# Kernel tuning notes

Measured on AMD Instinct MI355X. Metric: run time of the kernel, lower is better.

The kernel has to match this reference:

```python
import jax, jax.numpy as jnp
import numpy as np

EPS = 1e-5
NUM_HEADS = 4
HEAD_DIM = 64
NUM_STEPS = 3


def layernorm(x, g, b):
    mu = jnp.mean(x, axis=-1, keepdims=True)
    var = jnp.mean((x - mu) ** 2, axis=-1, keepdims=True)
    return (x - mu) / jnp.sqrt(var + EPS) * g + b


def entmax15(x):
    # exact alpha=1.5 entmax along last axis (Peters et al. 2019)
    n = x.shape[-1]
    x = x - jnp.max(x, axis=-1, keepdims=True)
    x = x / 2.0
    srt = -jnp.sort(-x, axis=-1)                      # descending
    rho = jnp.arange(1, n + 1, dtype=x.dtype)
    cs = jnp.cumsum(srt, axis=-1)
    cs2 = jnp.cumsum(srt * srt, axis=-1)
    mean = cs / rho
    ss = cs2 - mean * cs                              # k * (mean_sq - mean^2)
    delta = (1.0 - ss) / rho
    d = jnp.clip(delta, 0.0)
    safe = jnp.where(d > 0, d, 1.0)
    tau = mean - jnp.where(d > 0, jnp.sqrt(safe), 0.0)
    support = (tau <= srt).astype(jnp.int32)
    k_star = jnp.sum(support, axis=-1, keepdims=True) - 1
    tau_star = jnp.take_along_axis(tau, k_star, axis=-1)
    p = jnp.clip(x - tau_star, 0.0)
    return p * p


def setup_inputs() -> dict:
    key = jax.random.key(0)
    ks = jax.random.split(key, 8)
    B, S, Dh = 2, 512, 2048
    N, Dm = 8192, 1024
    T = NUM_HEADS * HEAD_DIM  # 256
    hidden = jax.random.normal(ks[0], (B, S, Dh), dtype=jnp.float32)
    memory = jax.random.normal(ks[1], (N, Dm), dtype=jnp.float32)
    Wq = jax.random.normal(ks[2], (Dh, T), dtype=jnp.float32) * 0.02
    Wk = jax.random.normal(ks[3], (Dm, T), dtype=jnp.float32) * 0.02
    Wv = jax.random.normal(ks[4], (Dm, T), dtype=jnp.float32) * 0.02
    Wo = jax.random.normal(ks[5], (T, Dh), dtype=jnp.float32) * 0.02
    log_beta = jnp.full((NUM_HEADS,), float(np.log(1.0 / np.sqrt(HEAD_DIM))), dtype=jnp.float32)
    g_s = jnp.ones((Dh,), jnp.float32)
    b_s = jnp.zeros((Dh,), jnp.float32)
    g_m = jnp.ones((Dm,), jnp.float32)
    b_m = jnp.zeros((Dm,), jnp.float32)
    return {"hidden": hidden, "memory": memory, "Wq": Wq, "Wk": Wk, "Wv": Wv,
            "Wo": Wo, "log_beta": log_beta, "g_s": g_s, "b_s": b_s,
            "g_m": g_m, "b_m": b_m}


def reference(hidden, memory, Wq, Wk, Wv, Wo, log_beta, g_s, b_s, g_m, b_m):
    B, S, _ = hidden.shape
    N = memory.shape[0]
    H, D = NUM_HEADS, HEAD_DIM
    Q = layernorm(hidden, g_s, b_s) @ Wq                         # [B,S,H*D]
    mem_n = layernorm(memory, g_m, b_m)
    K = (mem_n @ Wk).reshape(N, H, D).transpose(1, 0, 2)         # [H,N,D]
    V = (mem_n @ Wv).reshape(N, H, D).transpose(1, 0, 2)         # [H,N,D]
    xi = Q.reshape(B, S, H, D).transpose(0, 2, 1, 3)             # [B,H,S,D]
    beta = jnp.exp(log_beta)[None, :, None, None]                # [1,H,1,1]
    for _ in range(NUM_STEPS):
        scores = jnp.einsum('bhsd,hnd->bhsn', xi, K) * beta      # [B,H,S,N]
        w = entmax15(scores)
        xi = jnp.einsum('bhsn,hnd->bhsd', w, V)
    converged = xi.transpose(0, 2, 1, 3).reshape(B, S, H * D)
    output = converged @ Wo                                      # [B,S,hidden_dim]
    return output, converged
```

## Files before the change

kernel.cpp:

```cpp
#include <hip/hip_runtime.h>
#include <math.h>

typedef _Float16 f16;
typedef f16 f16x8 __attribute__((ext_vector_type(8)));
typedef float f32x4 __attribute__((ext_vector_type(4)));

#define QSCALE 16384.0f
#define QINV 6.103515625e-5f
#define QOFF 2.5f

__device__ __forceinline__ float wred_add(float v) {
#pragma unroll
  for (int off = 32; off >= 1; off >>= 1) v += __shfl_xor(v, off, 64);
  return v;
}
__device__ __forceinline__ float wred_max(float v) {
#pragma unroll
  for (int off = 32; off >= 1; off >>= 1) v = fmaxf(v, __shfl_xor(v, off, 64));
  return v;
}

__global__ __launch_bounds__(256) void ln_stats_all_kernel(
    const float* __restrict__ hidden, const float* __restrict__ memory,
    float* __restrict__ mu_h, float* __restrict__ rs_h,
    float* __restrict__ mu_m, float* __restrict__ rs_m) {
  int b = blockIdx.x, tid = threadIdx.x;
  const float* X;
  float* mu;
  float* rs;
  int cols, row;
  if (b < 1024) { X = hidden; cols = 2048; mu = mu_h; rs = rs_h; row = b; }
  else { X = memory; cols = 1024; mu = mu_m; rs = rs_m; row = b - 1024; }
  const float4* xr = (const float4*)(X + (size_t)row * cols);
  int nv = cols >> 10;
  float s = 0.f, s2 = 0.f;
  for (int v = 0; v < nv; ++v) {
    float4 x4 = xr[tid + (v << 8)];
    s += x4.x + x4.y + x4.z + x4.w;
    s2 += x4.x * x4.x + x4.y * x4.y + x4.z * x4.z + x4.w * x4.w;
  }
  s = wred_add(s);
  s2 = wred_add(s2);
  __shared__ float rb[8];
  int wid = tid >> 6, lane = tid & 63;
  if (lane == 0) { rb[wid] = s; rb[4 + wid] = s2; }
  __syncthreads();
  if (tid == 0) {
    float S = rb[0] + rb[1] + rb[2] + rb[3];
    float S2 = rb[4] + rb[5] + rb[6] + rb[7];
    float m = S / (float)cols;
    float var = S2 / (float)cols - m * m;
    mu[row] = m;
    rs[row] = 1.f / sqrtf(var + 1e-5f);
  }
}

__global__ __launch_bounds__(256) void split_a_kernel(
    const float* __restrict__ X, const float* __restrict__ mu,
    const float* __restrict__ rs, f16x8* __restrict__ Ah,
    f16x8* __restrict__ Al, int M, int Kd, int lay) {
  int blk = blockIdx.x * 4 + (threadIdx.x >> 6);
  int l = threadIdx.x & 63;
  int nmt = M >> 4;
  int kc = blk / nmt, mt = blk - kc * nmt;
  int m = mt * 16 + (l & 15);
  int k = kc * 32 + ((l >> 4) << 3);
  const float* src;
  if (lay == 0) {
    src = X + (size_t)m * Kd + k;
  } else {
    int b = m >> 9, s = m & 511, hh = k >> 6, d = k & 63;
    src = X + ((((size_t)b * 4 + hh) * 512 + s) << 6) + d;
  }
  float mm = mu ? mu[m] : 0.f;
  float rr = rs ? rs[m] : 1.f;
  f16x8 hi, lo;
#pragma unroll
  for (int j = 0; j < 8; ++j) {
    float v = (src[j] - mm) * rr;
    f16 hv = (f16)v;
    hi[j] = hv;
    lo[j] = (f16)((v - (float)hv) * 512.f);
  }
  size_t o = ((size_t)blk << 6) + l;
  Ah[o] = hi;
  Al[o] = lo;
}

__global__ __launch_bounds__(256) void split_w_all_kernel(
    const float* __restrict__ Wq, const float* __restrict__ Wk,
    const float* __restrict__ Wv, const float* __restrict__ Wo,
    const float* __restrict__ g_s, const float* __restrict__ g_m,
    f16x8* __restrict__ Bqh, f16x8* __restrict__ Bql,
    f16x8* __restrict__ Bkh, f16x8* __restrict__ Bkl,
    f16x8* __restrict__ Bvh, f16x8* __restrict__ Bvl,
    f16x8* __restrict__ Boh, f16x8* __restrict__ Bol) {
  int b = blockIdx.x;
  const float* W;
  const float* g;
  f16x8 *Bh, *Bl;
  int N, base;
  if (b < 256) { W = Wq; g = g_s; Bh = Bqh; Bl = Bql; N = 256; base = 0; }
  else if (b < 384) { W = Wk; g = g_m; Bh = Bkh; Bl = Bkl; N = 256; base = 256; }
  else if (b < 512) { W = Wv; g = g_m; Bh = Bvh; Bl = Bvl; N = 256; base = 384; }
  else { W = Wo; g = nullptr; Bh = Boh; Bl = Bol; N = 2048; base = 512; }
  int blk = (b - base) * 4 + (threadIdx.x >> 6);
  int l = threadIdx.x & 63;
  int nnt = N >> 4;
  int kc = blk / nnt, nt = blk - kc * nnt;
  int n = nt * 16 + (l & 15);
  int k0 = kc * 32 + ((l >> 4) << 3);
  f16x8 hi, lo;
#pragma unroll
  for (int j = 0; j < 8; ++j) {
    float v = W[(size_t)(k0 + j) * N + n];
    if (g) v *= g[k0 + j];
    f16 hv = (f16)v;
    hi[j] = hv;
    lo[j] = (f16)((v - (float)hv) * 512.f);
  }
  size_t o = ((size_t)blk << 6) + l;
  Bh[o] = hi;
  Bl[o] = lo;
}

__global__ __launch_bounds__(256) void wcol3_kernel(
    const float* __restrict__ Wq, const float* __restrict__ bq,
    const float* __restrict__ Wk, const float* __restrict__ bk,
    const float* __restrict__ Wv, const float* __restrict__ bv,
    float* __restrict__ vbq, float* __restrict__ vbk,
    float* __restrict__ vbv) {
  int which = blockIdx.z;
  const float* W = which == 0 ? Wq : (which == 1 ? Wk : Wv);
  const float* b = which == 0 ? bq : (which == 1 ? bk : bv);
  float* vb = which == 0 ? vbq : (which == 1 ? vbk : vbv);
  int Kd = which == 0 ? 2048 : 1024;
  int t = threadIdx.x;
  int kpb = Kd >> 4;
  int k0 = blockIdx.y * kpb;
  float s = 0.f;
  for (int k = k0; k < k0 + kpb; ++k) s = fmaf(b[k], W[(size_t)k * 256 + t], s);
  atomicAdd(&vb[t], s);
}

__global__ __launch_bounds__(256) void gemm_mfma_kernel(
    const f16x8* __restrict__ Ah, const f16x8* __restrict__ Al,
    const f16x8* __restrict__ Bh, const f16x8* __restrict__ Bl,
    const float* __restrict__ vb, float* __restrict__ outf,
    f16x8* __restrict__ o16a, f16x8* __restrict__ o16b, int M, int N, int nk,
    int out_mode) {
  __shared__ __align__(16) float Ts[64][68];
  const int tid = threadIdx.x;
  const int w = tid >> 6, l = tid & 63;
  const int ql = l & 15, g = l >> 4;
  const int bn = blockIdx.x, bm = blockIdx.y;
  const size_t astr = ((size_t)(M >> 4)) << 6;
  const size_t bstr = ((size_t)(N >> 4)) << 6;
  const f16x8* aph = Ah + (((size_t)(bm * 4 + w)) << 6) + l;
  const f16x8* apl = Al + (((size_t)(bm * 4 + w)) << 6) + l;
  const f16x8* bph = Bh + (((size_t)(bn * 4)) << 6) + l;
  const f16x8* bpl = Bl + (((size_t)(bn * 4)) << 6) + l;

  f32x4 cm[4], cx[4];
#pragma unroll
  for (int nf = 0; nf < 4; ++nf) {
    cm[nf] = (f32x4){0.f, 0.f, 0.f, 0.f};
    cx[nf] = (f32x4){0.f, 0.f, 0.f, 0.f};
  }

  f16x8 a0h = aph[0], a0l = apl[0];
  f16x8 b0h[4], b0l[4];
#pragma unroll
  for (int nf = 0; nf < 4; ++nf) {
    b0h[nf] = bph[nf << 6];
    b0l[nf] = bpl[nf << 6];
  }

  for (int kc = 0; kc < nk - 1; ++kc) {
    const size_t ao = (size_t)(kc + 1) * astr;
    const size_t bo = (size_t)(kc + 1) * bstr;
    f16x8 a1h = aph[ao], a1l = apl[ao];
    f16x8 b1h[4], b1l[4];
#pragma unroll
    for (int nf = 0; nf < 4; ++nf) {
      b1h[nf] = bph[bo + (nf << 6)];
      b1l[nf] = bpl[bo + (nf << 6)];
    }
#pragma unroll
    for (int nf = 0; nf < 4; ++nf) {
      cm[nf] = __builtin_amdgcn_mfma_f32_16x16x32_f16(a0h, b0h[nf], cm[nf], 0, 0, 0);
      cx[nf] = __builtin_amdgcn_mfma_f32_16x16x32_f16(a0h, b0l[nf], cx[nf], 0, 0, 0);
      cx[nf] = __builtin_amdgcn_mfma_f32_16x16x32_f16(a0l, b0h[nf], cx[nf], 0, 0, 0);
    }
    a0h = a1h;
    a0l = a1l;
#pragma unroll
    for (int nf = 0; nf < 4; ++nf) {
      b0h[nf] = b1h[nf];
      b0l[nf] = b1l[nf];
    }
  }
#pragma unroll
  for (int nf = 0; nf < 4; ++nf) {
    cm[nf] = __builtin_amdgcn_mfma_f32_16x16x32_f16(a0h, b0h[nf], cm[nf], 0, 0, 0);
    cx[nf] = __builtin_amdgcn_mfma_f32_16x16x32_f16(a0h, b0l[nf], cx[nf], 0, 0, 0);
    cx[nf] = __builtin_amdgcn_mfma_f32_16x16x32_f16(a0l, b0h[nf], cx[nf], 0, 0, 0);
  }

  float vbc[4] = {0.f, 0.f, 0.f, 0.f};
  if (vb) {
#pragma unroll
    for (int nf = 0; nf < 4; ++nf) vbc[nf] = vb[bn * 64 + nf * 16 + ql];
  }

  if (out_mode == 0) {
#pragma unroll
    for (int nf = 0; nf < 4; ++nf)
#pragma unroll
      for (int r = 0; r < 4; ++r) {
        float val = fmaf(cx[nf][r], 0.001953125f, cm[nf][r]) + vbc[nf];
        int m = bm * 64 + w * 16 + (g << 2) + r;
        int n = bn * 64 + nf * 16 + ql;
        int b = m >> 9, s = m & 511, hh = n >> 6, d = n & 63;
        outf[((((size_t)b * 4 + hh) * 512 + s) << 6) + d] = val;
      }
  } else if (out_mode == 3) {
#pragma unroll
    for (int nf = 0; nf < 4; ++nf)
#pragma unroll
      for (int r = 0; r < 4; ++r) {
        float val = fmaf(cx[nf][r], 0.001953125f, cm[nf][r]) + vbc[nf];
        int m = bm * 64 + w * 16 + (g << 2) + r;
        int n = bn * 64 + nf * 16 + ql;
        outf[(size_t)m * N + n] = val;
      }
  } else {
#pragma unroll
    for (int nf = 0; nf < 4; ++nf)
#pragma unroll
      for (int r = 0; r < 4; ++r)
        Ts[w * 16 + (g << 2) + r][nf * 16 + ql] =
            fmaf(cx[nf][r], 0.001953125f, cm[nf][r]) + vbc[nf];
    __syncthreads();
    if (out_mode == 4) {
#pragma unroll
      for (int i = 0; i < 2; ++i) {
        int slot = tid + (i << 8);
        int blk = slot >> 6, l2 = slot & 63;
        int ktl = blk >> 1, dc = blk & 1;
        int key = (ktl << 4) + (l2 & 15);
        int db = (dc << 5) + ((l2 >> 4) << 3);
        f16x8 hi, lo;
#pragma unroll
        for (int j = 0; j < 8; ++j) {
          float v = Ts[key][db + j];
          f16 hv = (f16)v;
          hi[j] = hv;
          lo[j] = (f16)((v - (float)hv) * 512.f);
        }
        size_t o = (((size_t)(bn * 512 + bm * 4 + ktl) * 2 + dc) << 6) + l2;
        o16a[o] = hi;
        o16b[o] = lo;
      }
    } else {
#pragma unroll
      for (int i = 0; i < 2; ++i) {
        int slot = tid + (i << 8);
        int blk = slot >> 6, l2 = slot & 63;
        int dt = blk >> 1, kcl = blk & 1;
        int keyb = (kcl << 5) + ((l2 >> 4) << 3);
        int d = (dt << 4) + (l2 & 15);
        f16x8 v8;
#pragma unroll
        for (int j = 0; j < 8; ++j) v8[j] = (f16)Ts[keyb + j][d];
        size_t o = (((size_t)(bn * 4 + dt) * 256 + bm * 2 + kcl) << 6) + l2;
        o16a[o] = v8;
      }
    }
  }
}

__global__ __launch_bounds__(512) void hop_score_kernel(
    const float* __restrict__ xi_in, const f16x8* __restrict__ Khi,
    const f16x8* __restrict__ Klo, const float* __restrict__ log_beta,
    unsigned short* __restrict__ Y) {
  __shared__ float xiq[16][64];
  __shared__ float mxb[8][16];
  __shared__ float mxs[16];
  const int tid = threadIdx.x;
  const int w = tid >> 6, l = tid & 63;
  const int ql = l & 15, g = l >> 4;
  const int bh = blockIdx.x & 7, qtile = blockIdx.x >> 3;
  const int h = bh & 3;
  const size_t base_io = ((size_t)bh * 512 + qtile * 16) * 64;

  float beta = expf(log_beta[h]);
  for (int i = tid; i < 1024; i += 512)
    xiq[i >> 6][i & 63] = xi_in[base_io + i] * beta;
  __syncthreads();

  f16x8 xh0, xh1, xl0, xl1;
#pragma unroll
  for (int j = 0; j < 8; ++j) {
    float x0 = xiq[ql][(g << 3) + j];
    float x1 = xiq[ql][32 + (g << 3) + j];
    f16 h0 = (f16)x0, h1 = (f16)x1;
    xh0[j] = h0; xl0[j] = (f16)((x0 - (float)h0) * 512.f);
    xh1[j] = h1; xl1[j] = (f16)((x1 - (float)h1) * 512.f);
  }

  const f16x8* kb = Khi + (size_t)h * 65536 + l;
  const f16x8* kl = Klo + (size_t)h * 65536 + l;
  const int kt0 = w * 64;

  float mymax = -3.4e38f;
  for (int kt = kt0; kt < kt0 + 2; ++kt) {
    f32x4 c = {0.f, 0.f, 0.f, 0.f};
    c = __builtin_amdgcn_mfma_f32_16x16x32_f16(kb[(size_t)kt * 128], xh0, c, 0, 0, 0);
    c = __builtin_amdgcn_mfma_f32_16x16x32_f16(kb[(size_t)kt * 128 + 64], xh1, c, 0, 0, 0);
    mymax = fmaxf(fmaxf(fmaxf(c[0], c[1]), fmaxf(c[2], c[3])), mymax);
  }
  mymax = fmaxf(mymax, __shfl_xor(mymax, 16, 64));
  mymax = fmaxf(mymax, __shfl_xor(mymax, 32, 64));
  if (l < 16) mxb[w][ql] = mymax;
  __syncthreads();
  if (tid < 16) {
    float m = mxb[0][tid];
#pragma unroll
    for (int ww = 1; ww < 8; ++ww) m = fmaxf(m, mxb[ww][tid]);
    mxs[tid] = m;
  }
  __syncthreads();
  const float mh = mxs[ql] * 0.5f;
  const float qc = QOFF * QSCALE + 0.5f - mh * QSCALE;

  const size_t Ybase = (size_t)(bh * 32 + qtile) * 131072;
  for (int kt = kt0; kt < kt0 + 64; ++kt) {
    f16x8 a0 = kb[(size_t)kt * 128], a1 = kb[(size_t)kt * 128 + 64];
    f16x8 b0 = kl[(size_t)kt * 128], b1 = kl[(size_t)kt * 128 + 64];
    f32x4 cm = {0.f, 0.f, 0.f, 0.f}, cx = {0.f, 0.f, 0.f, 0.f};
    cm = __builtin_amdgcn_mfma_f32_16x16x32_f16(a0, xh0, cm, 0, 0, 0);
    cm = __builtin_amdgcn_mfma_f32_16x16x32_f16(a1, xh1, cm, 0, 0, 0);
    cx = __builtin_amdgcn_mfma_f32_16x16x32_f16(b0, xh0, cx, 0, 0, 0);
    cx = __builtin_amdgcn_mfma_f32_16x16x32_f16(a0, xl0, cx, 0, 0, 0);
    cx = __builtin_amdgcn_mfma_f32_16x16x32_f16(b1, xh1, cx, 0, 0, 0);
    cx = __builtin_amdgcn_mfma_f32_16x16x32_f16(a1, xl1, cx, 0, 0, 0);
    ushort4 uv;
    unsigned short* up = (unsigned short*)&uv;
#pragma unroll
    for (int r = 0; r < 4; ++r) {
      float s = fmaf(cx[r], 0.001953125f, cm[r]);
      float uq = fmaf(s, 8192.0f, qc);
      uq = fminf(fmaxf(uq, 0.f), 65535.f);
      up[r] = (unsigned short)(int)uq;
    }
    *(ushort4*)&Y[Ybase + (size_t)(kt >> 1) * 512 + ql * 32 + (kt & 1) * 16 +
                  (g << 2)] = uv;
  }
}

#define TAU_EACH(OP)                                                        \
  OP(y0) OP(y1) OP(y2) OP(y3) OP(y4) OP(y5) OP(y6) OP(y7)                   \
  OP(y8) OP(y9) OP(y10) OP(y11) OP(y12) OP(y13) OP(y14) OP(y15)
#define OPMX(v) m = fmaxf(m, (v));
#define OPBI(v) { float d = fmaxf((v) - tv, 0.f); f = fmaf(d, d, f); }
#define OPRF(v)                                                             \
  { float d = fmaxf((v) - tc, 0.f);                                         \
    sd += d; sd2 = fmaf(d, d, sd2); cnt += (d > 0.f) ? 1.f : 0.f; }

__global__ __launch_bounds__(512, 2) void hop_tau_kernel(
    const unsigned short* __restrict__ Y, float* __restrict__ tau) {
  const int row = blockIdx.x;
  const int bh = row >> 9, qi = row & 511;
  const int qtile = qi >> 4, ql = qi & 15;
  const size_t yb = (size_t)(bh * 32 + qtile) * 131072 + ql * 32;
  const int t = threadIdx.x;
  const int wi = t >> 6, lane = t & 63;

  const uint4* p =
      (const uint4*)(Y + yb + (size_t)(t >> 1) * 512 + (t & 1) * 16);
  uint4 u0 = p[0], u1 = p[1];
  float y0 = fmaf((float)(u0.x & 0xffffu), QINV, -QOFF);
  float y1 = fmaf((float)(u0.x >> 16), QINV, -QOFF);
  float y2 = fmaf((float)(u0.y & 0xffffu), QINV, -QOFF);
  float y3 = fmaf((float)(u0.y >> 16), QINV, -QOFF);
  float y4 = fmaf((float)(u0.z & 0xffffu), QINV, -QOFF);
  float y5 = fmaf((float)(u0.z >> 16), QINV, -QOFF);
  float y6 = fmaf((float)(u0.w & 0xffffu), QINV, -QOFF);
  float y7 = fmaf((float)(u0.w >> 16), QINV, -QOFF);
  float y8 = fmaf((float)(u1.x & 0xffffu), QINV, -QOFF);
  float y9 = fmaf((float)(u1.x >> 16), QINV, -QOFF);
  float y10 = fmaf((float)(u1.y & 0xffffu), QINV, -QOFF);
  float y11 = fmaf((float)(u1.y >> 16), QINV, -QOFF);
  float y12 = fmaf((float)(u1.z & 0xffffu), QINV, -QOFF);
  float y13 = fmaf((float)(u1.z >> 16), QINV, -QOFF);
  float y14 = fmaf((float)(u1.w & 0xffffu), QINV, -QOFF);
  float y15 = fmaf((float)(u1.w >> 16), QINV, -QOFF);

  __shared__ float redm[8];
  __shared__ float rb[5][8];
  __shared__ float rb3[3][8][3];

  float m = y0;
  TAU_EACH(OPMX)
  m = wred_max(m);
  if (lane == 0) redm[wi] = m;
  __syncthreads();
  float ymax = redm[0];
#pragma unroll
  for (int s = 1; s < 8; ++s) ymax = fmaxf(ymax, redm[s]);

  float lo = ymax - 1.001f, hi = ymax;
#pragma unroll 1
  for (int it = 0; it < 5; ++it) {
    float tv = 0.5f * (lo + hi);
    float f = 0.f;
    TAU_EACH(OPBI)
    f = wred_add(f);
    if (lane == 0) rb[it][wi] = f;
    __syncthreads();
    float tot = 0.f;
#pragma unroll
    for (int s = 0; s < 8; ++s) tot += rb[it][s];
    if (tot >= 1.f) lo = tv; else hi = tv;
  }

  float tc = lo;
#pragma unroll 1
  for (int it = 0; it < 3; ++it) {
    float cnt = 0.f, sd = 0.f, sd2 = 0.f;
    TAU_EACH(OPRF)
    cnt = wred_add(cnt);
    sd = wred_add(sd);
    sd2 = wred_add(sd2);
    if (lane == 0) {
      rb3[it][wi][0] = cnt; rb3[it][wi][1] = sd; rb3[it][wi][2] = sd2;
    }
    __syncthreads();
    float K = 0.f, SD = 0.f, SD2 = 0.f;
#pragma unroll
    for (int s = 0; s < 8; ++s) {
      K += rb3[it][s][0]; SD += rb3[it][s][1]; SD2 += rb3[it][s][2];
    }
    if (K >= 0.5f) {
      float S1 = SD + K * tc;
      float S2 = SD2 + 2.f * tc * S1 - tc * tc * K;
      float mean = S1 / K;
      float ss = fmaf(-mean, S1, S2);
      float delta = (1.f - ss) / K;
      tc = delta > 0.f ? mean - sqrtf(delta) : mean;
    }
  }
  if (t == 0) tau[row] = tc;
}

__global__ __launch_bounds__(512) void hop_pv_kernel(
    const unsigned short* __restrict__ Y, const f16x8* __restrict__ Vp,
    const float* __restrict__ tau, float* __restrict__ xi_out) {
  __shared__ float outp[8][16][64];
  __shared__ float taus[16];
  const int tid = threadIdx.x;
  const int w = tid >> 6, l = tid & 63;
  const int ql = l & 15, g = l >> 4;
  const int bh = blockIdx.x & 7, qtile = blockIdx.x >> 3;
  const int h = bh & 3;
  const size_t base_io = ((size_t)bh * 512 + qtile * 16) * 64;

  if (tid < 16) taus[tid] = tau[bh * 512 + qtile * 16 + tid];
  __syncthreads();
  const float t1 = taus[ql];
  const size_t Ybase = (size_t)(bh * 32 + qtile) * 131072;
  const f16x8* vb = Vp + (size_t)h * 65536 + l;

  f32x4 m2[4];
#pragma unroll
  for (int dt = 0; dt < 4; ++dt) m2[dt] = (f32x4){0.f, 0.f, 0.f, 0.f};

  for (int kc = 0; kc < 32; ++kc) {
    const int chunk = w * 32 + kc;
    uint4 uv = *(const uint4*)(Y + Ybase + (size_t)chunk * 512 + ql * 32 +
                               (g << 3));
    unsigned a[4] = {uv.x, uv.y, uv.z, uv.w};
    f16x8 a2;
#pragma unroll
    for (int e = 0; e < 4; ++e) {
      float y0 = fmaf((float)(a[e] & 0xffffu), QINV, -QOFF);
      float y1 = fmaf((float)(a[e] >> 16), QINV, -QOFF);
      float p0 = fmaxf(y0 - t1, 0.f);
      float p1 = fmaxf(y1 - t1, 0.f);
      a2[e * 2] = (f16)(p0 * p0);
      a2[e * 2 + 1] = (f16)(p1 * p1);
    }
#pragma unroll
    for (int dt = 0; dt < 4; ++dt) {
      f16x8 vf = vb[(((size_t)dt * 256 + chunk) << 6)];
      m2[dt] = __builtin_amdgcn_mfma_f32_16x16x32_f16(a2, vf, m2[dt], 0, 0, 0);
    }
  }
#pragma unroll
  for (int dt = 0; dt < 4; ++dt)
#pragma unroll
    for (int r = 0; r < 4; ++r)
      outp[w][(g << 2) + r][dt * 16 + ql] = m2[dt][r];
  __syncthreads();
  for (int i = tid; i < 1024; i += 512) {
    float s = 0.f;
#pragma unroll
    for (int ww = 0; ww < 8; ++ww) s += outp[ww][i >> 6][i & 63];
    xi_out[base_io + i] = s;
  }
}

__global__ __launch_bounds__(256) void conv_copy_kernel(
    const float* __restrict__ xi, float* __restrict__ out) {
  int o4 = blockIdx.x * 256 + threadIdx.x;
  int o = o4 << 2;
  int dd = o & 63, hq = (o >> 6) & 3, sq = (o >> 8) & 511, bq = o >> 17;
  float4 v =
      *(const float4*)&xi[((((size_t)bq << 2) + hq) * 512 + sq) * 64 + dd];
  *(float4*)&out[o] = v;
}

extern "C" void kernel_launch(void* const* d_in, const int* in_sizes, int n_in,
                              void* d_out, int out_size, void* d_ws,
                              size_t ws_size, hipStream_t stream) {
  (void)in_sizes; (void)n_in; (void)out_size; (void)ws_size;
  const float* hidden = (const float*)d_in[0];
  const float* memory = (const float*)d_in[1];
  const float* Wq = (const float*)d_in[2];
  const float* Wk = (const float*)d_in[3];
  const float* Wv = (const float*)d_in[4];
  const float* Wo = (const float*)d_in[5];
  const float* log_beta = (const float*)d_in[6];
  const float* g_s = (const float*)d_in[7];
  const float* b_s = (const float*)d_in[8];
  const float* g_m = (const float*)d_in[9];
  const float* b_m = (const float*)d_in[10];
  float* out = (float*)d_out;

  float* ws = (float*)d_ws;
  float* mu_h = ws;
  float* rs_h = ws + 1024;
  float* mu_m = ws + 2048;
  float* rs_m = ws + 10240;
  float* xiA = ws + 18432;
  float* xiB = ws + 280576;
  float* vb_q = ws + 542720;
  float* vb_k = ws + 542976;
  float* vb_v = ws + 543232;
  float* tau = ws + 543488;
  f16x8* Khi = (f16x8*)(ws + 548864);
  f16x8* Klo = Khi + 262144;
  f16x8* Vp = Klo + 262144;
  f16x8* Bqh = Vp + 262144;
  f16x8* Bql = Bqh + 65536;
  f16x8* Bkh = Bql + 65536;
  f16x8* Bkl = Bkh + 32768;
  f16x8* Bvh = Bkl + 32768;
  f16x8* Bvl = Bvh + 32768;
  f16x8* Boh = Bvl + 32768;
  f16x8* Bol = Boh + 65536;
  unsigned short* Y = (unsigned short*)(Bol + 65536);
  f16x8* Amh = (f16x8*)Y;
  f16x8* Aml = Amh + 1048576;
  f16x8* Ahh = Aml + 1048576;
  f16x8* Ahl = Ahh + 262144;
  f16x8* Axh = Ahl + 262144;
  f16x8* Axl = Axh + 32768;

  ln_stats_all_kernel<<<9216, 256, 0, stream>>>(hidden, memory, mu_h, rs_h,
                                                mu_m, rs_m);
  hipMemsetAsync(vb_q, 0, 3 * 256 * sizeof(float), stream);

  split_a_kernel<<<1024, 256, 0, stream>>>(hidden, mu_h, rs_h, Ahh, Ahl, 1024,
                                           2048, 0);
  split_a_kernel<<<4096, 256, 0, stream>>>(memory, mu_m, rs_m, Amh, Aml, 8192,
                                           1024, 0);
  split_w_all_kernel<<<768, 256, 0, stream>>>(Wq, Wk, Wv, Wo, g_s, g_m, Bqh,
                                              Bql, Bkh, Bkl, Bvh, Bvl, Boh,
                                              Bol);
  wcol3_kernel<<<dim3(1, 16, 3), 256, 0, stream>>>(Wq, b_s, Wk, b_m, Wv, b_m,
                                                   vb_q, vb_k, vb_v);

  gemm_mfma_kernel<<<dim3(4, 16), 256, 0, stream>>>(
      Ahh, Ahl, Bqh, Bql, vb_q, xiA, nullptr, nullptr, 1024, 256, 64, 0);
  gemm_mfma_kernel<<<dim3(4, 128), 256, 0, stream>>>(
      Amh, Aml, Bkh, Bkl, vb_k, nullptr, Khi, Klo, 8192, 256, 32, 4);
  gemm_mfma_kernel<<<dim3(4, 128), 256, 0, stream>>>(
      Amh, Aml, Bvh, Bvl, vb_v, nullptr, Vp, nullptr, 8192, 256, 32, 5);

  float* xin = xiA;
  float* xout = xiB;
  for (int step = 0; step < 3; ++step) {
    hop_score_kernel<<<256, 512, 0, stream>>>(xin, Khi, Klo, log_beta, Y);
    hop_tau_kernel<<<4096, 512, 0, stream>>>(Y, tau);
    hop_pv_kernel<<<256, 512, 0, stream>>>(Y, Vp, tau, xout);
    float* t = xin; xin = xout; xout = t;
  }

  split_a_kernel<<<128, 256, 0, stream>>>(xin, nullptr, nullptr, Axh, Axl,
                                          1024, 256, 1);
  gemm_mfma_kernel<<<dim3(32, 16), 256, 0, stream>>>(
      Axh, Axl, Boh, Bol, nullptr, out, nullptr, nullptr, 1024, 2048, 8, 3);
  conv_copy_kernel<<<256, 256, 0, stream>>>(xin, out + 2097152);
}
```

Baseline: 499.3 us.

## Compact entmax tau candidates into LDS and iterate only over them

The tau kernel now uses 256 threads with 32 quantized scores each. It finds the max in integer space, then compacts only the scores within the possible support window (above max minus about 1) into shared memory with a prefix sum. The bisection and refinement iterations then loop over that small candidate list instead of all 8192 values. If more than 2048 candidates survive, it falls back to a full register scan. This adds a scan, an extra barrier and LDS use per block.

```diff
diff --git a/kernel.cpp b/kernel.cpp
--- a/kernel.cpp
+++ b/kernel.cpp
@@ -359,16 +359,7 @@
   }
 }
 
-#define TAU_EACH(OP)                                                        \
-  OP(y0) OP(y1) OP(y2) OP(y3) OP(y4) OP(y5) OP(y6) OP(y7)                   \
-  OP(y8) OP(y9) OP(y10) OP(y11) OP(y12) OP(y13) OP(y14) OP(y15)
-#define OPMX(v) m = fmaxf(m, (v));
-#define OPBI(v) { float d = fmaxf((v) - tv, 0.f); f = fmaf(d, d, f); }
-#define OPRF(v)                                                             \
-  { float d = fmaxf((v) - tc, 0.f);                                         \
-    sd += d; sd2 = fmaf(d, d, sd2); cnt += (d > 0.f) ? 1.f : 0.f; }
-
-__global__ __launch_bounds__(512, 2) void hop_tau_kernel(
+__global__ __launch_bounds__(256) void hop_tau_kernel(
     const unsigned short* __restrict__ Y, float* __restrict__ tau) {
   const int row = blockIdx.x;
   const int bh = row >> 9, qi = row & 511;
@@ -377,80 +368,156 @@
   const int t = threadIdx.x;
   const int wi = t >> 6, lane = t & 63;
 
-  const uint4* p =
-      (const uint4*)(Y + yb + (size_t)(t >> 1) * 512 + (t & 1) * 16);
-  uint4 u0 = p[0], u1 = p[1];
-  float y0 = fmaf((float)(u0.x & 0xffffu), QINV, -QOFF);
-  float y1 = fmaf((float)(u0.x >> 16), QINV, -QOFF);
-  float y2 = fmaf((float)(u0.y & 0xffffu), QINV, -QOFF);
-  float y3 = fmaf((float)(u0.y >> 16), QINV, -QOFF);
-  float y4 = fmaf((float)(u0.z & 0xffffu), QINV, -QOFF);
-  float y5 = fmaf((float)(u0.z >> 16), QINV, -QOFF);
-  float y6 = fmaf((float)(u0.w & 0xffffu), QINV, -QOFF);
-  float y7 = fmaf((float)(u0.w >> 16), QINV, -QOFF);
-  float y8 = fmaf((float)(u1.x & 0xffffu), QINV, -QOFF);
-  float y9 = fmaf((float)(u1.x >> 16), QINV, -QOFF);
-  float y10 = fmaf((float)(u1.y & 0xffffu), QINV, -QOFF);
-  float y11 = fmaf((float)(u1.y >> 16), QINV, -QOFF);
-  float y12 = fmaf((float)(u1.z & 0xffffu), QINV, -QOFF);
-  float y13 = fmaf((float)(u1.z >> 16), QINV, -QOFF);
-  float y14 = fmaf((float)(u1.w & 0xffffu), QINV, -QOFF);
-  float y15 = fmaf((float)(u1.w >> 16), QINV, -QOFF);
-
-  __shared__ float redm[8];
-  __shared__ float rb[5][8];
-  __shared__ float rb3[3][8][3];
-
-  float m = y0;
-  TAU_EACH(OPMX)
-  m = wred_max(m);
-  if (lane == 0) redm[wi] = m;
-  __syncthreads();
-  float ymax = redm[0];
-#pragma unroll
-  for (int s = 1; s < 8; ++s) ymax = fmaxf(ymax, redm[s]);
-
-  float lo = ymax - 1.001f, hi = ymax;
+  __shared__ float cand[2048];
+  __shared__ int wsum[4];
+  __shared__ unsigned redu[4];
+  __shared__ float rbf[5][4];
+  __shared__ float rb3[3][4][3];
+
+  const uint4* p = (const uint4*)(Y + yb + (size_t)t * 512);
+  uint4 q0 = p[0], q1 = p[1], q2 = p[2], q3 = p[3];
+
+#define TAU_DWORDS(OP)                                                      \
+  OP(q0.x) OP(q0.y) OP(q0.z) OP(q0.w) OP(q1.x) OP(q1.y) OP(q1.z) OP(q1.w)   \
+  OP(q2.x) OP(q2.y) OP(q2.z) OP(q2.w) OP(q3.x) OP(q3.y) OP(q3.z) OP(q3.w)
+
+  unsigned um = 0;
+#define OPMAXU(w) { unsigned a = (w) & 0xffffu, b = (w) >> 16;              \
+                    if (a > um) um = a; if (b > um) um = b; }
+  TAU_DWORDS(OPMAXU)
+#undef OPMAXU
+#pragma unroll
+  for (int off = 32; off >= 1; off >>= 1) {
+    unsigned o = (unsigned)__shfl_xor((int)um, off, 64);
+    if (o > um) um = o;
+  }
+  if (lane == 0) redu[wi] = um;
+  __syncthreads();
+  unsigned umax = redu[0];
+  if (redu[1] > umax) umax = redu[1];
+  if (redu[2] > umax) umax = redu[2];
+  if (redu[3] > umax) umax = redu[3];
+  const float ymax = fmaf((float)umax, QINV, -QOFF);
+  const float lo0 = ymax - 1.001f;
+  const int uthr = (int)umax - 16401;
+
+  int c = 0;
+#define OPCNT(w) { if ((int)((w) & 0xffffu) > uthr) ++c;                    \
+                   if ((int)((w) >> 16) > uthr) ++c; }
+  TAU_DWORDS(OPCNT)
+#undef OPCNT
+  int inc = c;
+#pragma unroll
+  for (int off = 1; off < 64; off <<= 1) {
+    int v2 = __shfl_up(inc, off, 64);
+    if (lane >= off) inc += v2;
+  }
+  if (lane == 63) wsum[wi] = inc;
+  __syncthreads();
+  int base = inc - c;
+#pragma unroll
+  for (int s = 0; s < 4; ++s)
+    if (s < wi) base += wsum[s];
+  const int total = wsum[0] + wsum[1] + wsum[2] + wsum[3];
+
+  float tc;
+  if (total <= 2048) {
+    int idx = base;
+#define OPPUT(w) { int a = (int)((w) & 0xffffu);                            \
+                   if (a > uthr) cand[idx++] = fmaf((float)a, QINV, -QOFF); \
+                   int b = (int)((w) >> 16);                                \
+                   if (b > uthr) cand[idx++] = fmaf((float)b, QINV, -QOFF); }
+    TAU_DWORDS(OPPUT)
+#undef OPPUT
+    __syncthreads();
+
+    float lo = lo0, hi = ymax;
 #pragma unroll 1
-  for (int it = 0; it < 5; ++it) {
-    float tv = 0.5f * (lo + hi);
-    float f = 0.f;
-    TAU_EACH(OPBI)
-    f = wred_add(f);
-    if (lane == 0) rb[it][wi] = f;
-    __syncthreads();
-    float tot = 0.f;
-#pragma unroll
-    for (int s = 0; s < 8; ++s) tot += rb[it][s];
-    if (tot >= 1.f) lo = tv; else hi = tv;
-  }
-
-  float tc = lo;
+    for (int it = 0; it < 5; ++it) {
+      float tv = 0.5f * (lo + hi);
+      float f = 0.f;
+      for (int i = t; i < total; i += 256) {
+        float d = fmaxf(cand[i] - tv, 0.f);
+        f = fmaf(d, d, f);
+      }
+      f = wred_add(f);
+      if (lane == 0) rbf[it][wi] = f;
+      __syncthreads();
+      float tot = rbf[it][0] + rbf[it][1] + rbf[it][2] + rbf[it][3];
+      if (tot >= 1.f) lo = tv; else hi = tv;
+    }
+    tc = lo;
 #pragma unroll 1
-  for (int it = 0; it < 3; ++it) {
-    float cnt = 0.f, sd = 0.f, sd2 = 0.f;
-    TAU_EACH(OPRF)
-    cnt = wred_add(cnt);
-    sd = wred_add(sd);
-    sd2 = wred_add(sd2);
-    if (lane == 0) {
-      rb3[it][wi][0] = cnt; rb3[it][wi][1] = sd; rb3[it][wi][2] = sd2;
-    }
-    __syncthreads();
-    float K = 0.f, SD = 0.f, SD2 = 0.f;
-#pragma unroll
-    for (int s = 0; s < 8; ++s) {
-      K += rb3[it][s][0]; SD += rb3[it][s][1]; SD2 += rb3[it][s][2];
-    }
-    if (K >= 0.5f) {
-      float S1 = SD + K * tc;
-      float S2 = SD2 + 2.f * tc * S1 - tc * tc * K;
-      float mean = S1 / K;
-      float ss = fmaf(-mean, S1, S2);
-      float delta = (1.f - ss) / K;
-      tc = delta > 0.f ? mean - sqrtf(delta) : mean;
-    }
-  }
+    for (int it = 0; it < 3; ++it) {
+      float kk = 0.f, s1 = 0.f, s2 = 0.f;
+      for (int i = t; i < total; i += 256) {
+        float yy = cand[i];
+        if (yy > tc) { kk += 1.f; s1 += yy; s2 = fmaf(yy, yy, s2); }
+      }
+      kk = wred_add(kk);
+      s1 = wred_add(s1);
+      s2 = wred_add(s2);
+      if (lane == 0) {
+        rb3[it][wi][0] = kk; rb3[it][wi][1] = s1; rb3[it][wi][2] = s2;
+      }
+      __syncthreads();
+      float K = rb3[it][0][0] + rb3[it][1][0] + rb3[it][2][0] + rb3[it][3][0];
+      float S1 = rb3[it][0][1] + rb3[it][1][1] + rb3[it][2][1] + rb3[it][3][1];
+      float S2 = rb3[it][0][2] + rb3[it][1][2] + rb3[it][2][2] + rb3[it][3][2];
+      if (K >= 0.5f) {
+        float mean = S1 / K;
+        float ss = fmaf(-mean, S1, S2);
+        float delta = (1.f - ss) / K;
+        tc = delta > 0.f ? mean - sqrtf(delta) : mean;
+      }
+    }
+  } else {
+    float lo = lo0, hi = ymax;
+#pragma unroll 1
+    for (int it = 0; it < 5; ++it) {
+      float tv = 0.5f * (lo + hi);
+      float f = 0.f;
+#define OPBI(w) { float ya = fmaf((float)((w) & 0xffffu), QINV, -QOFF);     \
+                  float yd = fmaxf(ya - tv, 0.f); f = fmaf(yd, yd, f);      \
+                  float yb2 = fmaf((float)((w) >> 16), QINV, -QOFF);        \
+                  float ye = fmaxf(yb2 - tv, 0.f); f = fmaf(ye, ye, f); }
+      TAU_DWORDS(OPBI)
+#undef OPBI
+      f = wred_add(f);
+      if (lane == 0) rbf[it][wi] = f;
+      __syncthreads();
+      float tot = rbf[it][0] + rbf[it][1] + rbf[it][2] + rbf[it][3];
+      if (tot >= 1.f) lo = tv; else hi = tv;
+    }
+    tc = lo;
+#pragma unroll 1
+    for (int it = 0; it < 3; ++it) {
+      float kk = 0.f, s1 = 0.f, s2 = 0.f;
+#define OPRF(w) { float ya = fmaf((float)((w) & 0xffffu), QINV, -QOFF);     \
+                  if (ya > tc) { kk += 1.f; s1 += ya; s2 = fmaf(ya, ya, s2); } \
+                  float yb2 = fmaf((float)((w) >> 16), QINV, -QOFF);        \
+                  if (yb2 > tc) { kk += 1.f; s1 += yb2; s2 = fmaf(yb2, yb2, s2); } }
+      TAU_DWORDS(OPRF)
+#undef OPRF
+      kk = wred_add(kk);
+      s1 = wred_add(s1);
+      s2 = wred_add(s2);
+      if (lane == 0) {
+        rb3[it][wi][0] = kk; rb3[it][wi][1] = s1; rb3[it][wi][2] = s2;
+      }
+      __syncthreads();
+      float K = rb3[it][0][0] + rb3[it][1][0] + rb3[it][2][0] + rb3[it][3][0];
+      float S1 = rb3[it][0][1] + rb3[it][1][1] + rb3[it][2][1] + rb3[it][3][1];
+      float S2 = rb3[it][0][2] + rb3[it][1][2] + rb3[it][2][2] + rb3[it][3][2];
+      if (K >= 0.5f) {
+        float mean = S1 / K;
+        float ss = fmaf(-mean, S1, S2);
+        float delta = (1.f - ss) / K;
+        tc = delta > 0.f ? mean - sqrtf(delta) : mean;
+      }
+    }
+  }
+#undef TAU_DWORDS
   if (t == 0) tau[row] = tc;
 }
 
@@ -593,7 +660,7 @@
   float* xout = xiB;
   for (int step = 0; step < 3; ++step) {
     hop_score_kernel<<<256, 512, 0, stream>>>(xin, Khi, Klo, log_beta, Y);
-    hop_tau_kernel<<<4096, 512, 0, stream>>>(Y, tau);
+    hop_tau_kernel<<<4096, 256, 0, stream>>>(Y, tau);
     hop_pv_kernel<<<256, 512, 0, stream>>>(Y, Vp, tau, xout);
     float* t = xin; xin = xout; xout = t;
   }
```

New measurement: 467.1 us. 1.07x faster.
